# Kernel tuning notes

Hardware: AMD Instinct MI355X
Metric: run time of the kernel (lower is better)

Reference implementation:

```python
import jax, jax.numpy as jnp
import numpy as np

APP_DIM = 27
FEA_PE = 6
VIEW_PE = 6
FEATURE_C = 128
DENSITY_SHIFT = -10.0
DISTANCE_SCALE = 25.0
IN_MLPC = 2 * VIEW_PE * 3 + 2 * FEA_PE * APP_DIM + 3 + APP_DIM  # 390


def positional_encoding(x, freqs):
    # x: [..., C] -> [..., 2*freqs*C]
    freq_bands = (2.0 ** jnp.arange(freqs)).astype(x.dtype)
    pts = (x[..., None] * freq_bands).reshape(x.shape[:-1] + (freqs * x.shape[-1],))
    return jnp.concatenate([jnp.sin(pts), jnp.cos(pts)], axis=-1)


def alpha2weights(alpha):
    # alpha: [N_rays, N_samples]; last sample forced opaque (as in source)
    alpha = alpha.at[:, -1].set(1.0)
    trans = jnp.concatenate(
        [jnp.ones((alpha.shape[0], 1), alpha.dtype), 1.0 - alpha + 1e-10], axis=-1)
    T = jnp.cumprod(trans, axis=-1)
    weights = alpha * T[:, :-1]
    return weights, T


def setup_inputs() -> dict:
    key = jax.random.key(0)
    ks = jax.random.split(key, 12)
    N_rays, N_samples = 4096, 128
    sigma_feat = jax.random.normal(ks[0], (N_rays, N_samples), jnp.float32)
    app_features = 0.1 * jax.random.normal(ks[1], (N_rays, N_samples, APP_DIM), jnp.float32)
    vd = jax.random.normal(ks[2], (N_rays, N_samples, 3), jnp.float32)
    viewdirs = vd / (jnp.linalg.norm(vd, axis=-1, keepdims=True) + 1e-8)
    dists = 0.02 * jax.random.uniform(ks[3], (N_rays, N_samples), jnp.float32)

    def linear(k, fan_in, fan_out):
        kw, kb = jax.random.split(k)
        lim = 1.0 / np.sqrt(fan_in)
        W = jax.random.uniform(kw, (fan_in, fan_out), jnp.float32, -lim, lim)
        b = jax.random.uniform(kb, (fan_out,), jnp.float32, -lim, lim)
        return W, b

    W1, b1 = linear(ks[4], IN_MLPC, FEATURE_C)
    W2, b2 = linear(ks[5], FEATURE_C, FEATURE_C)
    W3, _ = linear(ks[6], FEATURE_C, 3)
    b3 = jnp.zeros((3,), jnp.float32)  # bias of last layer initialized to 0 in source
    return {"sigma_feat": sigma_feat, "app_features": app_features,
            "viewdirs": viewdirs, "dists": dists,
            "W1": W1, "b1": b1, "W2": W2, "b2": b2, "W3": W3, "b3": b3}


def reference(sigma_feat, app_features, viewdirs, dists, W1, b1, W2, b2, W3, b3):
    # feature2density: softplus with density_shift
    sigma = jax.nn.softplus(sigma_feat + DENSITY_SHIFT)
    alpha = 1.0 - jnp.exp(-sigma * dists * DISTANCE_SCALE)  # [N_rays, N_samples]
    weights, _T = alpha2weights(alpha)

    # MLPRender_Fea: cat[features, viewdirs, PE(features), PE(viewdirs)]
    mlp_in = jnp.concatenate(
        [app_features, viewdirs,
         positional_encoding(app_features, FEA_PE),
         positional_encoding(viewdirs, VIEW_PE)], axis=-1)  # [R, S, 390]
    h = jax.nn.relu(jnp.einsum('rsc,cf->rsf', mlp_in, W1) + b1)
    h = jax.nn.relu(jnp.einsum('rsf,fg->rsg', h, W2) + b2)
    rgb = jax.nn.sigmoid(jnp.einsum('rsg,go->rso', h, W3) + b3)  # [R, S, 3]

    rgb_map = jnp.sum(weights[..., None] * rgb, axis=-2)  # [R, 3]
    return rgb_map
```

## Files before the change

### kernel.cpp

```cpp
#include <hip/hip_runtime.h>
#include <math.h>

typedef unsigned short u16;
using bf16x8 = __attribute__((ext_vector_type(8))) short;
using f32x4  = __attribute__((ext_vector_type(4))) float;

#define NS      128
#define NBLOCKS 4096
#define NSLICE  19
#define OWGT    81920

#define POOLSZ 32768
#define OH2    16384

#define BAR() do { asm volatile("s_waitcnt lgkmcnt(0)" ::: "memory");        \
                   __builtin_amdgcn_s_barrier();                              \
                   asm volatile("" ::: "memory"); } while (0)

#define MF(A,B,C) __builtin_amdgcn_mfma_f32_16x16x32_bf16((A),(B),(C),0,0,0)

__device__ __forceinline__ u16 f2bf(float f) {
    unsigned int i = __float_as_uint(f);
    return (u16)((i + 0x7FFFu + ((i >> 16) & 1u)) >> 16);
}

__device__ __forceinline__ unsigned pk(float hi, float lo) {
    unsigned r;
    asm("v_cvt_pk_bf16_f32 %0, %1, %2" : "=v"(r) : "v"(lo), "v"(hi));
    return r;
}

__device__ __forceinline__ int afoff_h(int m, int k) {
    int chunk = ((k >> 5) * 8 + (m >> 4)) * 64 + ((k >> 3) & 3) * 16 + (m & 15);
    chunk ^= (k >> 3) & 3;
    return chunk * 8 + (k & 7);
}

__device__ __forceinline__ int orig_k(int ch, int slot) {
    if (ch < 27) {
        if (slot == 0) return ch;
        if (slot <= 6) return 30 + ch * 6 + (slot - 1);
        return 192 + ch * 6 + (slot - 7);
    } else {
        int c = ch - 27;
        if (slot == 0) return 27 + c;
        if (slot <= 6) return 354 + c * 6 + (slot - 1);
        return 372 + c * 6 + (slot - 7);
    }
}

__device__ __forceinline__ float ldch(const float* ap, const float* vp, int c) {
    return (c < 27) ? ap[c] : vp[c - 27];
}

__device__ __forceinline__ void build_x(u16* dst, float v) {
    float rev = v * 0.15915494309189535f;
    rev -= floorf(rev);
    float s0 = __builtin_amdgcn_sinf(rev);
    float c0 = __builtin_amdgcn_cosf(rev);
    float s1 = 2.f * s0 * c0, c1 = c0 * c0 - s0 * s0;
    float s2 = 2.f * s1 * c1, c2 = c1 * c1 - s1 * s1;
    float s3 = 2.f * s2 * c2, c3 = c2 * c2 - s2 * s2;
    float s4 = 2.f * s3 * c3, c4 = c3 * c3 - s3 * s3;
    float s5 = 2.f * s4 * c4, c5 = c4 * c4 - s4 * s4;
    uint4 lo, hi;
    lo.x = pk(s0, v);  lo.y = pk(s2, s1);  lo.z = pk(s4, s3);  lo.w = pk(c0, s5);
    hi.x = pk(c2, c1); hi.y = pk(c4, c3);  hi.z = pk(0.f, c5); hi.w = 0u;
    *(uint4*)(dst)       = lo;
    *(uint4*)(dst + 128) = hi;
}

__global__ __launch_bounds__(256) void prep_kernel(
    const float* __restrict__ W1, const float* __restrict__ W2,
    const float* __restrict__ W3, const float* __restrict__ sigma_g,
    const float* __restrict__ dists_g, u16* __restrict__ ws,
    float* __restrict__ out)
{
    int idx = blockIdx.x * 256 + threadIdx.x;
    if (idx < 12288) out[idx] = 0.f;
    if (idx < 61440) {
        int j = idx & 7, lane = (idx >> 3) & 63, nt = (idx >> 9) & 7, ks = idx >> 12;
        int q = lane >> 4, l15 = lane & 15;
        int klocal = q * 8 + j;
        int ch = ks * 2 + (klocal >> 4);
        int slot = klocal & 15;
        int n = nt * 16 + l15;
        ws[idx] = (slot < 13) ? f2bf(W1[orig_k(ch, slot) * 128 + n]) : (u16)0;
    } else if (idx < 77824) {
        int i2 = idx - 61440;
        int j = i2 & 7, lane = (i2 >> 3) & 63, nt = (i2 >> 9) & 7, ks = i2 >> 12;
        int k = ks * 32 + (lane >> 4) * 8 + j;
        int n = nt * 16 + (lane & 15);
        ws[idx] = f2bf(W2[k * 128 + n]);
    } else if (idx < 79872) {
        int i3 = idx - 77824;
        int j = i3 & 7, lane = (i3 >> 3) & 63, ks = i3 >> 9;
        int k = ks * 32 + (lane >> 4) * 8 + j;
        int n = lane & 15;
        ws[idx] = (n < 3) ? f2bf(W3[k * 3 + n]) : (u16)0;
    }
    {
        int ray = idx >> 6, ln = idx & 63;
        float* wgt = (float*)(ws + OWGT);
        int base = ray * NS;
        float x0 = sigma_g[base + ln] - 10.f;
        float sp0 = (x0 > 20.f) ? x0 : log1pf(expf(x0));
        float a0 = 1.f - expf(-sp0 * dists_g[base + ln] * 25.f);
        float x1 = sigma_g[base + 64 + ln] - 10.f;
        float sp1 = (x1 > 20.f) ? x1 : log1pf(expf(x1));
        float a1 = 1.f - expf(-sp1 * dists_g[base + 64 + ln] * 25.f);
        if (ln == 63) a1 = 1.f;
        float p0 = 1.f - a0 + 1e-10f;
        float p1 = 1.f - a1 + 1e-10f;
        #pragma unroll
        for (int d = 1; d < 64; d <<= 1) {
            float v0 = __shfl_up(p0, d);
            float v1 = __shfl_up(p1, d);
            if (ln >= d) { p0 *= v0; p1 *= v1; }
        }
        float S0 = __shfl(p0, 63);
        float q0 = __shfl_up(p0, 1);
        float q1 = __shfl_up(p1, 1);
        wgt[base + ln]      = a0 * ((ln == 0) ? 1.f : q0);
        wgt[base + 64 + ln] = a1 * ((ln == 0) ? 1.f : q1) * S0;
    }
}

#define LOADB2(N0, N1, s)                                                     \
    if ((s) < NSLICE) {                                                       \
        const u16* wp = wp0 + (s) * 4096;                                     \
        N0 = *(const bf16x8*)(wp);                                            \
        N1 = *(const bf16x8*)(wp + 512);                                      \
    }

#define BODYX(s, C0,C1, N0,N1)                                                \
  {                                                                           \
    LOADB2(N0, N1, (s)+2);                                                    \
    const u16* ab = pool + ((s)&7)*4096 + (wm*256 + lane)*8;                  \
    bf16x8 a0 = *(const bf16x8*)(ab);                                         \
    bf16x8 a1 = *(const bf16x8*)(ab + 512);                                   \
    __builtin_amdgcn_s_setprio(1);                                            \
    acc[0][0]=MF(a0,C0,acc[0][0]); acc[0][1]=MF(a0,C1,acc[0][1]);             \
    acc[1][0]=MF(a1,C0,acc[1][0]); acc[1][1]=MF(a1,C1,acc[1][1]);             \
    a0 = *(const bf16x8*)(ab + 1024);                                         \
    a1 = *(const bf16x8*)(ab + 1536);                                         \
    acc[2][0]=MF(a0,C0,acc[2][0]); acc[2][1]=MF(a0,C1,acc[2][1]);             \
    acc[3][0]=MF(a1,C0,acc[3][0]); acc[3][1]=MF(a1,C1,acc[3][1]);             \
    __builtin_amdgcn_s_setprio(0);                                            \
  }

#define BODYX0(s, C0,C1, N0,N1)                                               \
  {                                                                           \
    LOADB2(N0, N1, (s)+2);                                                    \
    const u16* ab = pool + ((s)&7)*4096 + (wm*256 + lane)*8;                  \
    bf16x8 a0 = *(const bf16x8*)(ab);                                         \
    bf16x8 a1 = *(const bf16x8*)(ab + 512);                                   \
    __builtin_amdgcn_s_setprio(1);                                            \
    acc[0][0]=MF(a0,C0,vzero); acc[0][1]=MF(a0,C1,vzero);                     \
    acc[1][0]=MF(a1,C0,vzero); acc[1][1]=MF(a1,C1,vzero);                     \
    a0 = *(const bf16x8*)(ab + 1024);                                         \
    a1 = *(const bf16x8*)(ab + 1536);                                         \
    acc[2][0]=MF(a0,C0,vzero); acc[2][1]=MF(a0,C1,vzero);                     \
    acc[3][0]=MF(a1,C0,vzero); acc[3][1]=MF(a1,C1,vzero);                     \
    __builtin_amdgcn_s_setprio(0);                                            \
  }

#define BODYH(s, C0,C1, N0,N1)                                                \
  {                                                                           \
    LOADB2(N0, N1, (s)+2);                                                    \
    int cb = ((((s)-15)*512) + wm*256 + lane) ^ quad;                         \
    bf16x8 a0 = *(const bf16x8*)(pool + cb*8);                                \
    bf16x8 a1 = *(const bf16x8*)(pool + (cb+64)*8);                           \
    __builtin_amdgcn_s_setprio(1);                                            \
    acc[0][0]=MF(a0,C0,acc[0][0]); acc[0][1]=MF(a0,C1,acc[0][1]);             \
    acc[1][0]=MF(a1,C0,acc[1][0]); acc[1][1]=MF(a1,C1,acc[1][1]);             \
    a0 = *(const bf16x8*)(pool + (cb+128)*8);                                 \
    a1 = *(const bf16x8*)(pool + (cb+192)*8);                                 \
    acc[2][0]=MF(a0,C0,acc[2][0]); acc[2][1]=MF(a0,C1,acc[2][1]);             \
    acc[3][0]=MF(a1,C0,acc[3][0]); acc[3][1]=MF(a1,C1,acc[3][1]);             \
    __builtin_amdgcn_s_setprio(0);                                            \
  }

#define BODYH0(s, C0,C1, N0,N1)                                               \
  {                                                                           \
    LOADB2(N0, N1, (s)+2);                                                    \
    int cb = ((((s)-15)*512) + wm*256 + lane) ^ quad;                         \
    bf16x8 a0 = *(const bf16x8*)(pool + cb*8);                                \
    bf16x8 a1 = *(const bf16x8*)(pool + (cb+64)*8);                           \
    __builtin_amdgcn_s_setprio(1);                                            \
    acc[0][0]=MF(a0,C0,vzero); acc[0][1]=MF(a0,C1,vzero);                     \
    acc[1][0]=MF(a1,C0,vzero); acc[1][1]=MF(a1,C1,vzero);                     \
    a0 = *(const bf16x8*)(pool + (cb+128)*8);                                 \
    a1 = *(const bf16x8*)(pool + (cb+192)*8);                                 \
    acc[2][0]=MF(a0,C0,vzero); acc[2][1]=MF(a0,C1,vzero);                     \
    acc[3][0]=MF(a1,C0,vzero); acc[3][1]=MF(a1,C1,vzero);                     \
    __builtin_amdgcn_s_setprio(0);                                            \
  }

#define GENDQ(p)                                                              \
  {                                                                           \
    if (8*(p)+8  + cl < 30)                                                   \
        build_x(pool + ((2*(p)+2)&3)*8192 + (cl>>1)*4096 + bxoff, pv_a);      \
    if (8*(p)+12 + cl < 30)                                                   \
        build_x(pool + ((2*(p)+3)&3)*8192 + (cl>>1)*4096 + bxoff, pv_b);      \
    pv_a = pv_c; pv_b = pv_d;                                                 \
    if (8*(p)+24 + cl < 30) pv_c = ldch(ap, vp, 8*(p)+24 + cl);               \
    if (8*(p)+28 + cl < 30) pv_d = ldch(ap, vp, 8*(p)+28 + cl);               \
    BAR();                                                                    \
  }

#define EPI4(OFS, ACC, BB, rwb, col)                                          \
  { f32x4 t_ = ACC + BB;                                                      \
    t_ = __builtin_elementwise_max(t_, vzero);                                \
    unsigned w01_ = pk(t_[1], t_[0]);                                         \
    unsigned w23_ = pk(t_[3], t_[2]);                                         \
    pool[(OFS) + afoff_h((rwb) + 0, col)] = (u16)w01_;                        \
    pool[(OFS) + afoff_h((rwb) + 1, col)] = (u16)(w01_ >> 16);                \
    pool[(OFS) + afoff_h((rwb) + 2, col)] = (u16)w23_;                        \
    pool[(OFS) + afoff_h((rwb) + 3, col)] = (u16)(w23_ >> 16); }

__global__ __launch_bounds__(512, 4) void render_kernel(
    const float* __restrict__ app_g,   const float* __restrict__ view_g,
    const float* __restrict__ b1_g,    const float* __restrict__ b2_g,
    const float* __restrict__ b3_g,    const u16* __restrict__ ws,
    float* __restrict__ out_g)
{
    __shared__ __align__(16) u16 pool[POOLSZ];

    const int tid  = threadIdx.x;
    const int lane = tid & 63;
    const int wave = tid >> 6;
    const int l15  = lane & 15;
    const int quad = lane >> 4;
    const int wm   = wave >> 2;
    const int wn   = wave & 3;

    const int r  = blockIdx.x;
    const int rb = r * NS;
    const int row = tid & 127;
    const int cl  = tid >> 7;
    const float* ap = app_g  + (rb + row) * 27;
    const float* vp = view_g + (rb + row) * 3;
    const int bxoff = (row >> 4) * 512 + (((cl & 1) * 32) + (row & 15)) * 8;

    const u16* wp0 = ws + (wn * 128 + lane) * 8;
    bf16x8 bP0, bP1, bQ0, bQ1, bR0, bR1;
    LOADB2(bP0, bP1, 0);
    LOADB2(bQ0, bQ1, 1);

    float pv_a = ldch(ap, vp, cl);
    float pv_b = ldch(ap, vp, 4 + cl);
    float pv_c = ldch(ap, vp, 8 + cl);
    float pv_d = ldch(ap, vp, 12 + cl);

    build_x(pool +        (cl >> 1) * 4096 + bxoff, pv_a);
    build_x(pool + 8192 + (cl >> 1) * 4096 + bxoff, pv_b);
    pv_a = pv_c; pv_b = pv_d;
    pv_c = ldch(ap, vp, 16 + cl);
    pv_d = ldch(ap, vp, 20 + cl);
    BAR();

    const f32x4 vzero = {0.f, 0.f, 0.f, 0.f};
    f32x4 acc[4][2];

    BODYX0(0, bP0,bP1, bR0,bR1);
    BODYX(1,  bQ0,bQ1, bP0,bP1);
    BODYX(2,  bR0,bR1, bQ0,bQ1);
    BODYX(3,  bP0,bP1, bR0,bR1);  GENDQ(0);
    BODYX(4,  bQ0,bQ1, bP0,bP1);
    BODYX(5,  bR0,bR1, bQ0,bQ1);
    BODYX(6,  bP0,bP1, bR0,bR1);
    BODYX(7,  bQ0,bQ1, bP0,bP1);  GENDQ(1);
    BODYX(8,  bR0,bR1, bQ0,bQ1);
    BODYX(9,  bP0,bP1, bR0,bR1);
    BODYX(10, bQ0,bQ1, bP0,bP1);
    BODYX(11, bR0,bR1, bQ0,bQ1);  GENDQ(2);
    const float b1r0 = b1_g[wn * 32 + l15];
    const float b1r1 = b1_g[wn * 32 + 16 + l15];
    BODYX(12, bP0,bP1, bR0,bR1);
    BODYX(13, bQ0,bQ1, bP0,bP1);
    BODYX(14, bR0,bR1, bQ0,bQ1);

    {
        const f32x4 bb0 = {b1r0, b1r0, b1r0, b1r0};
        const f32x4 bb1 = {b1r1, b1r1, b1r1, b1r1};
        #pragma unroll
        for (int mt = 0; mt < 4; ++mt) {
            int rwb = wm * 64 + mt * 16 + quad * 4;
            EPI4(0, acc[mt][0], bb0, rwb, wn * 32 + l15);
            EPI4(0, acc[mt][1], bb1, rwb, wn * 32 + 16 + l15);
        }
    }
    BAR();

    const float b2r0 = b2_g[wn * 32 + l15];
    const float b2r1 = b2_g[wn * 32 + 16 + l15];

    BODYH0(15, bP0,bP1, bR0,bR1);
    BODYH(16, bQ0,bQ1, bP0,bP1);
    BODYH(17, bR0,bR1, bQ0,bQ1);
    BODYH(18, bP0,bP1, bR0,bR1);

    {
        const f32x4 bb0 = {b2r0, b2r0, b2r0, b2r0};
        const f32x4 bb1 = {b2r1, b2r1, b2r1, b2r1};
        #pragma unroll
        for (int mt = 0; mt < 4; ++mt) {
            int rwb = wm * 64 + mt * 16 + quad * 4;
            EPI4(OH2, acc[mt][0], bb0, rwb, wn * 32 + l15);
            EPI4(OH2, acc[mt][1], bb1, rwb, wn * 32 + 16 + l15);
        }
    }
    BAR();

    const u16* w3r = ws + 77824;
    const float4 w4 = *(const float4*)((const float*)(ws + OWGT)
                                       + rb + wave * 16 + quad * 4);
    const float b3v = (l15 < 3) ? b3_g[l15] : 0.f;
    f32x4 acc3 = vzero;
    #pragma unroll
    for (int ks = 0; ks < 4; ++ks) {
        bf16x8 w3f = *(const bf16x8*)(w3r + (ks * 64 + lane) * 8);
        int c = ((ks * 8 + wave) * 64 + lane) ^ quad;
        bf16x8 a3 = *(const bf16x8*)(pool + OH2 + c * 8);
        acc3 = MF(a3, w3f, acc3);
    }
    float v = 0.f;
    if (l15 < 3) {
        v  = w4.x / (1.f + expf(-(acc3[0] + b3v)));
        v += w4.y / (1.f + expf(-(acc3[1] + b3v)));
        v += w4.z / (1.f + expf(-(acc3[2] + b3v)));
        v += w4.w / (1.f + expf(-(acc3[3] + b3v)));
    }
    v += __shfl_xor(v, 16);
    v += __shfl_xor(v, 32);
    if (lane < 3)
        atomicAdd(&out_g[r * 3 + lane], v);
}

extern "C" void kernel_launch(void* const* d_in, const int* in_sizes, int n_in,
                              void* d_out, int out_size, void* d_ws, size_t ws_size,
                              hipStream_t stream) {
    (void)in_sizes; (void)n_in; (void)out_size; (void)ws_size;
    const float* sigma = (const float*)d_in[0];
    const float* app   = (const float*)d_in[1];
    const float* view  = (const float*)d_in[2];
    const float* dists = (const float*)d_in[3];
    const float* W1    = (const float*)d_in[4];
    const float* b1    = (const float*)d_in[5];
    const float* W2    = (const float*)d_in[6];
    const float* b2    = (const float*)d_in[7];
    const float* W3    = (const float*)d_in[8];
    const float* b3    = (const float*)d_in[9];
    float* out = (float*)d_out;

    u16* ws = (u16*)d_ws;

    prep_kernel<<<1024, 256, 0, stream>>>(W1, W2, W3, sigma, dists, ws, out);
    render_kernel<<<NBLOCKS, 512, 0, stream>>>(app, view, b1, b2, b3, ws, out);
}
```

Baseline: 192.9 us.

## Process four rays per block with cross-ray prefetch of inputs and weights

Turns the kernel into a persistent-style loop where each block handles four consecutive rays instead of one, launching a quarter as many blocks. The next ray's feature and viewdir loads are issued mid-way through the current ray's first GEMM, and the next x tile is built in shared memory after the final layer. This amortizes block launch and prologue cost and overlaps global loads with MFMA work. In exchange there are fewer blocks (1024) for load balance across CUs, plus an extra barrier per ray. Correctness depends on the macros still reading pv_* and pool state consistently across iterations.

After: 375.5 us. 94.6% more time.

```diff
diff --git a/kernel.cpp b/kernel.cpp
--- a/kernel.cpp
+++ b/kernel.cpp
@@ -6,7 +6,8 @@
 using f32x4  = __attribute__((ext_vector_type(4))) float;
 
 #define NS      128
-#define NBLOCKS 4096
+#define RPB     4
+#define NBLOCKS (4096 / RPB)
 #define NSLICE  19
 #define OWGT    81920
 
@@ -235,13 +236,12 @@
     const int wm   = wave >> 2;
     const int wn   = wave & 3;
 
-    const int r  = blockIdx.x;
-    const int rb = r * NS;
-    const int row = tid & 127;
-    const int cl  = tid >> 7;
-    const float* ap = app_g  + (rb + row) * 27;
-    const float* vp = view_g + (rb + row) * 3;
-    const int bxoff = (row >> 4) * 512 + (((cl & 1) * 32) + (row & 15)) * 8;
+    const int r0  = blockIdx.x * RPB;
+    const int rowl = tid & 127;
+    const int cl   = tid >> 7;
+    const float* ap = app_g  + (r0 * NS + rowl) * 27;
+    const float* vp = view_g + (r0 * NS + rowl) * 3;
+    const int bxoff = (rowl >> 4) * 512 + (((cl & 1) * 32) + (rowl & 15)) * 8;
 
     const u16* wp0 = ws + (wn * 128 + lane) * 8;
     bf16x8 bP0, bP1, bQ0, bQ1, bR0, bR1;
@@ -261,81 +261,103 @@
     BAR();
 
     const f32x4 vzero = {0.f, 0.f, 0.f, 0.f};
+    const u16* w3r = ws + 77824;
+    const float b3v = (l15 < 3) ? b3_g[l15] : 0.f;
     f32x4 acc[4][2];
 
-    BODYX0(0, bP0,bP1, bR0,bR1);
-    BODYX(1,  bQ0,bQ1, bP0,bP1);
-    BODYX(2,  bR0,bR1, bQ0,bQ1);
-    BODYX(3,  bP0,bP1, bR0,bR1);  GENDQ(0);
-    BODYX(4,  bQ0,bQ1, bP0,bP1);
-    BODYX(5,  bR0,bR1, bQ0,bQ1);
-    BODYX(6,  bP0,bP1, bR0,bR1);
-    BODYX(7,  bQ0,bQ1, bP0,bP1);  GENDQ(1);
-    BODYX(8,  bR0,bR1, bQ0,bQ1);
-    BODYX(9,  bP0,bP1, bR0,bR1);
-    BODYX(10, bQ0,bQ1, bP0,bP1);
-    BODYX(11, bR0,bR1, bQ0,bQ1);  GENDQ(2);
-    const float b1r0 = b1_g[wn * 32 + l15];
-    const float b1r1 = b1_g[wn * 32 + 16 + l15];
-    BODYX(12, bP0,bP1, bR0,bR1);
-    BODYX(13, bQ0,bQ1, bP0,bP1);
-    BODYX(14, bR0,bR1, bQ0,bQ1);
-
-    {
-        const f32x4 bb0 = {b1r0, b1r0, b1r0, b1r0};
-        const f32x4 bb1 = {b1r1, b1r1, b1r1, b1r1};
+    #pragma unroll 1
+    for (int ri = 0; ri < RPB; ++ri) {
+        BODYX0(0, bP0,bP1, bR0,bR1);
+        BODYX(1,  bQ0,bQ1, bP0,bP1);
+        BODYX(2,  bR0,bR1, bQ0,bQ1);
+        BODYX(3,  bP0,bP1, bR0,bR1);  GENDQ(0);
+        BODYX(4,  bQ0,bQ1, bP0,bP1);
+        BODYX(5,  bR0,bR1, bQ0,bQ1);
+        BODYX(6,  bP0,bP1, bR0,bR1);
+        BODYX(7,  bQ0,bQ1, bP0,bP1);  GENDQ(1);
+        BODYX(8,  bR0,bR1, bQ0,bQ1);
+        BODYX(9,  bP0,bP1, bR0,bR1);
+        BODYX(10, bQ0,bQ1, bP0,bP1);
+        BODYX(11, bR0,bR1, bQ0,bQ1);  GENDQ(2);
+
+        if (ri + 1 < RPB) {
+            ap += NS * 27; vp += NS * 3;
+            pv_a = ldch(ap, vp, cl);
+            pv_b = ldch(ap, vp, 4 + cl);
+            pv_c = ldch(ap, vp, 8 + cl);
+            pv_d = ldch(ap, vp, 12 + cl);
+        }
+        const float b1r0 = b1_g[wn * 32 + l15];
+        const float b1r1 = b1_g[wn * 32 + 16 + l15];
+        BODYX(12, bP0,bP1, bR0,bR1);
+        BODYX(13, bQ0,bQ1, bP0,bP1);
+        BODYX(14, bR0,bR1, bQ0,bQ1);
+
+        {
+            const f32x4 bb0 = {b1r0, b1r0, b1r0, b1r0};
+            const f32x4 bb1 = {b1r1, b1r1, b1r1, b1r1};
+            #pragma unroll
+            for (int mt = 0; mt < 4; ++mt) {
+                int rwb = wm * 64 + mt * 16 + quad * 4;
+                EPI4(0, acc[mt][0], bb0, rwb, wn * 32 + l15);
+                EPI4(0, acc[mt][1], bb1, rwb, wn * 32 + 16 + l15);
+            }
+        }
+        BAR();
+
+        const float b2r0 = b2_g[wn * 32 + l15];
+        const float b2r1 = b2_g[wn * 32 + 16 + l15];
+
+        BODYH0(15, bP0,bP1, bR0,bR1);
+        BODYH(16, bQ0,bQ1, bP0,bP1);
+        BODYH(17, bR0,bR1, bQ0,bQ1);
+        BODYH(18, bP0,bP1, bR0,bR1);
+
+        {
+            const f32x4 bb0 = {b2r0, b2r0, b2r0, b2r0};
+            const f32x4 bb1 = {b2r1, b2r1, b2r1, b2r1};
+            #pragma unroll
+            for (int mt = 0; mt < 4; ++mt) {
+                int rwb = wm * 64 + mt * 16 + quad * 4;
+                EPI4(OH2, acc[mt][0], bb0, rwb, wn * 32 + l15);
+                EPI4(OH2, acc[mt][1], bb1, rwb, wn * 32 + 16 + l15);
+            }
+        }
+        BAR();
+
+        const float4 w4 = *(const float4*)((const float*)(ws + OWGT)
+                          + (r0 + ri) * NS + wave * 16 + quad * 4);
+        f32x4 acc3 = vzero;
         #pragma unroll
-        for (int mt = 0; mt < 4; ++mt) {
-            int rwb = wm * 64 + mt * 16 + quad * 4;
-            EPI4(0, acc[mt][0], bb0, rwb, wn * 32 + l15);
-            EPI4(0, acc[mt][1], bb1, rwb, wn * 32 + 16 + l15);
-        }
-    }
-    BAR();
-
-    const float b2r0 = b2_g[wn * 32 + l15];
-    const float b2r1 = b2_g[wn * 32 + 16 + l15];
-
-    BODYH0(15, bP0,bP1, bR0,bR1);
-    BODYH(16, bQ0,bQ1, bP0,bP1);
-    BODYH(17, bR0,bR1, bQ0,bQ1);
-    BODYH(18, bP0,bP1, bR0,bR1);
-
-    {
-        const f32x4 bb0 = {b2r0, b2r0, b2r0, b2r0};
-        const f32x4 bb1 = {b2r1, b2r1, b2r1, b2r1};
-        #pragma unroll
-        for (int mt = 0; mt < 4; ++mt) {
-            int rwb = wm * 64 + mt * 16 + quad * 4;
-            EPI4(OH2, acc[mt][0], bb0, rwb, wn * 32 + l15);
-            EPI4(OH2, acc[mt][1], bb1, rwb, wn * 32 + 16 + l15);
-        }
-    }
-    BAR();
-
-    const u16* w3r = ws + 77824;
-    const float4 w4 = *(const float4*)((const float*)(ws + OWGT)
-                                       + rb + wave * 16 + quad * 4);
-    const float b3v = (l15 < 3) ? b3_g[l15] : 0.f;
-    f32x4 acc3 = vzero;
-    #pragma unroll
-    for (int ks = 0; ks < 4; ++ks) {
-        bf16x8 w3f = *(const bf16x8*)(w3r + (ks * 64 + lane) * 8);
-        int c = ((ks * 8 + wave) * 64 + lane) ^ quad;
-        bf16x8 a3 = *(const bf16x8*)(pool + OH2 + c * 8);
-        acc3 = MF(a3, w3f, acc3);
-    }
-    float v = 0.f;
-    if (l15 < 3) {
-        v  = w4.x / (1.f + expf(-(acc3[0] + b3v)));
-        v += w4.y / (1.f + expf(-(acc3[1] + b3v)));
-        v += w4.z / (1.f + expf(-(acc3[2] + b3v)));
-        v += w4.w / (1.f + expf(-(acc3[3] + b3v)));
-    }
-    v += __shfl_xor(v, 16);
-    v += __shfl_xor(v, 32);
-    if (lane < 3)
-        atomicAdd(&out_g[r * 3 + lane], v);
+        for (int ks = 0; ks < 4; ++ks) {
+            bf16x8 w3f = *(const bf16x8*)(w3r + (ks * 64 + lane) * 8);
+            int c = ((ks * 8 + wave) * 64 + lane) ^ quad;
+            bf16x8 a3 = *(const bf16x8*)(pool + OH2 + c * 8);
+            acc3 = MF(a3, w3f, acc3);
+        }
+        if (ri + 1 < RPB) {
+            LOADB2(bP0, bP1, 0);
+            LOADB2(bQ0, bQ1, 1);
+            build_x(pool +        (cl >> 1) * 4096 + bxoff, pv_a);
+            build_x(pool + 8192 + (cl >> 1) * 4096 + bxoff, pv_b);
+            pv_a = pv_c; pv_b = pv_d;
+            pv_c = ldch(ap, vp, 16 + cl);
+            pv_d = ldch(ap, vp, 20 + cl);
+        }
+        float v = 0.f;
+        if (l15 < 3) {
+            v  = w4.x / (1.f + expf(-(acc3[0] + b3v)));
+            v += w4.y / (1.f + expf(-(acc3[1] + b3v)));
+            v += w4.z / (1.f + expf(-(acc3[2] + b3v)));
+            v += w4.w / (1.f + expf(-(acc3[3] + b3v)));
+        }
+        v += __shfl_xor(v, 16);
+        v += __shfl_xor(v, 32);
+        if (lane < 3)
+            atomicAdd(&out_g[(r0 + ri) * 3 + lane], v);
+
+        if (ri + 1 < RPB) BAR();
+    }
 }
 
 extern "C" void kernel_launch(void* const* d_in, const int* in_sizes, int n_in,
```

## Process two rays per block with cross-ray prefetch of inputs and weights

Applied to the files above, without the earlier changes.

Each block now handles two rays in sequence instead of one, halving the grid. While the first ray is still in its later layers, the block prefetches the second ray's input features and weight fragments and builds its first encoded input tiles. This hides per-block startup latency and overlaps it with the previous ray's epilogue. The cost is more register pressure and half as many blocks, which leaves fewer blocks to balance across CUs.

Measured after the change: 235.0 us. 21.8% more time.

```diff
diff --git a/kernel.cpp b/kernel.cpp
--- a/kernel.cpp
+++ b/kernel.cpp
@@ -6,7 +6,8 @@
 using f32x4  = __attribute__((ext_vector_type(4))) float;
 
 #define NS      128
-#define NBLOCKS 4096
+#define RPB     2
+#define NBLOCKS (4096 / RPB)
 #define NSLICE  19
 #define OWGT    81920
 
@@ -219,6 +220,95 @@
     pool[(OFS) + afoff_h((rwb) + 2, col)] = (u16)w23_;                        \
     pool[(OFS) + afoff_h((rwb) + 3, col)] = (u16)(w23_ >> 16); }
 
+#define RAY(RI, PREF)                                                         \
+  {                                                                           \
+    BODYX0(0, bP0,bP1, bR0,bR1);                              \
+    BODYX(1,  bQ0,bQ1, bP0,bP1);                                              \
+    BODYX(2,  bR0,bR1, bQ0,bQ1);                                              \
+    BODYX(3,  bP0,bP1, bR0,bR1);  GENDQ(0);           \
+    BODYX(4,  bQ0,bQ1, bP0,bP1);                                              \
+    BODYX(5,  bR0,bR1, bQ0,bQ1);                                              \
+    BODYX(6,  bP0,bP1, bR0,bR1);                                              \
+    BODYX(7,  bQ0,bQ1, bP0,bP1);  GENDQ(1);          \
+    BODYX(8,  bR0,bR1, bQ0,bQ1);                                              \
+    BODYX(9,  bP0,bP1, bR0,bR1);                                              \
+    BODYX(10, bQ0,bQ1, bP0,bP1);                                              \
+    BODYX(11, bR0,bR1, bQ0,bQ1);  GENDQ(2);         \
+    if (PREF) {   \
+        ap += NS * 27; vp += NS * 3;                                          \
+        pv_a = ldch(ap, vp, cl);                                              \
+        pv_b = ldch(ap, vp, 4 + cl);                                          \
+        pv_c = ldch(ap, vp, 8 + cl);                                          \
+        pv_d = ldch(ap, vp, 12 + cl);                                         \
+    }                                                                         \
+    const float b1r0 = b1_g[wn * 32 + l15];                                   \
+    const float b1r1 = b1_g[wn * 32 + 16 + l15];                              \
+    BODYX(12, bP0,bP1, bR0,bR1);                                              \
+    BODYX(13, bQ0,bQ1, bP0,bP1);                     \
+    BODYX(14, bR0,bR1, bQ0,bQ1);                     \
+        \
+    {                                                                         \
+        const f32x4 bb0 = {b1r0, b1r0, b1r0, b1r0};                           \
+        const f32x4 bb1 = {b1r1, b1r1, b1r1, b1r1};                           \
+        _Pragma("unroll")                                                     \
+        for (int mt = 0; mt < 4; ++mt) {                                      \
+            int rwb = wm * 64 + mt * 16 + quad * 4;                           \
+            EPI4(0, acc[mt][0], bb0, rwb, wn * 32 + l15);                     \
+            EPI4(0, acc[mt][1], bb1, rwb, wn * 32 + 16 + l15);                \
+        }                                                                     \
+    }                                                                         \
+    BAR();                           \
+    const float b2r0 = b2_g[wn * 32 + l15];                                   \
+    const float b2r1 = b2_g[wn * 32 + 16 + l15];                              \
+    BODYH0(15, bP0,bP1, bR0,bR1);              \
+    BODYH(16, bQ0,bQ1, bP0,bP1);                     \
+    BODYH(17, bR0,bR1, bQ0,bQ1);                                              \
+    BODYH(18, bP0,bP1, bR0,bR1);                                              \
+        \
+    {                                                                         \
+        const f32x4 bb0 = {b2r0, b2r0, b2r0, b2r0};                           \
+        const f32x4 bb1 = {b2r1, b2r1, b2r1, b2r1};                           \
+        _Pragma("unroll")                                                     \
+        for (int mt = 0; mt < 4; ++mt) {                                      \
+            int rwb = wm * 64 + mt * 16 + quad * 4;                           \
+            EPI4(OH2, acc[mt][0], bb0, rwb, wn * 32 + l15);                   \
+            EPI4(OH2, acc[mt][1], bb1, rwb, wn * 32 + 16 + l15);              \
+        }                                                                     \
+    }                                                                         \
+    BAR();                  \
+       \
+    const float4 w4 = *(const float4*)((const float*)(ws + OWGT)              \
+                      + (r0 + (RI)) * NS + wave * 16 + quad * 4);             \
+    f32x4 acc3 = vzero;                                                       \
+    _Pragma("unroll")                                                         \
+    for (int ks = 0; ks < 4; ++ks) {                                          \
+        bf16x8 w3f = *(const bf16x8*)(w3r + (ks * 64 + lane) * 8);            \
+        int c = ((ks * 8 + wave) * 64 + lane) ^ quad;                         \
+        bf16x8 a3 = *(const bf16x8*)(pool + OH2 + c * 8);                     \
+        acc3 = MF(a3, w3f, acc3);                                             \
+    }                                                                         \
+    if (PREF) {                                                               \
+        LOADB2(bP0, bP1, 0);                  \
+        LOADB2(bQ0, bQ1, 1);                                                  \
+        build_x(pool +        (cl >> 1) * 4096 + bxoff, pv_a);                \
+        build_x(pool + 8192 + (cl >> 1) * 4096 + bxoff, pv_b);                \
+        pv_a = pv_c; pv_b = pv_d;                                             \
+        pv_c = ldch(ap, vp, 16 + cl);                                 \
+        pv_d = ldch(ap, vp, 20 + cl);                                 \
+    }                                                                         \
+    float v = 0.f;                                                            \
+    if (l15 < 3) {                                                            \
+        v  = w4.x / (1.f + expf(-(acc3[0] + b3v)));                           \
+        v += w4.y / (1.f + expf(-(acc3[1] + b3v)));                           \
+        v += w4.z / (1.f + expf(-(acc3[2] + b3v)));                           \
+        v += w4.w / (1.f + expf(-(acc3[3] + b3v)));                           \
+    }                                                                         \
+    v += __shfl_xor(v, 16);                                                   \
+    v += __shfl_xor(v, 32);                                                   \
+    if (lane < 3)                                                             \
+        atomicAdd(&out_g[(r0 + (RI)) * 3 + lane], v);                         \
+  }
+
 __global__ __launch_bounds__(512, 4) void render_kernel(
     const float* __restrict__ app_g,   const float* __restrict__ view_g,
     const float* __restrict__ b1_g,    const float* __restrict__ b2_g,
@@ -235,13 +325,12 @@
     const int wm   = wave >> 2;
     const int wn   = wave & 3;
 
-    const int r  = blockIdx.x;
-    const int rb = r * NS;
-    const int row = tid & 127;
-    const int cl  = tid >> 7;
-    const float* ap = app_g  + (rb + row) * 27;
-    const float* vp = view_g + (rb + row) * 3;
-    const int bxoff = (row >> 4) * 512 + (((cl & 1) * 32) + (row & 15)) * 8;
+    const int r0  = blockIdx.x * RPB;
+    const int rowl = tid & 127;
+    const int cl   = tid >> 7;
+    const float* ap = app_g  + (r0 * NS + rowl) * 27;
+    const float* vp = view_g + (r0 * NS + rowl) * 3;
+    const int bxoff = (rowl >> 4) * 512 + (((cl & 1) * 32) + (rowl & 15)) * 8;
 
     const u16* wp0 = ws + (wn * 128 + lane) * 8;
     bf16x8 bP0, bP1, bQ0, bQ1, bR0, bR1;
@@ -261,81 +350,13 @@
     BAR();
 
     const f32x4 vzero = {0.f, 0.f, 0.f, 0.f};
+    const u16* w3r = ws + 77824;
+    const float b3v = (l15 < 3) ? b3_g[l15] : 0.f;
     f32x4 acc[4][2];
 
-    BODYX0(0, bP0,bP1, bR0,bR1);
-    BODYX(1,  bQ0,bQ1, bP0,bP1);
-    BODYX(2,  bR0,bR1, bQ0,bQ1);
-    BODYX(3,  bP0,bP1, bR0,bR1);  GENDQ(0);
-    BODYX(4,  bQ0,bQ1, bP0,bP1);
-    BODYX(5,  bR0,bR1, bQ0,bQ1);
-    BODYX(6,  bP0,bP1, bR0,bR1);
-    BODYX(7,  bQ0,bQ1, bP0,bP1);  GENDQ(1);
-    BODYX(8,  bR0,bR1, bQ0,bQ1);
-    BODYX(9,  bP0,bP1, bR0,bR1);
-    BODYX(10, bQ0,bQ1, bP0,bP1);
-    BODYX(11, bR0,bR1, bQ0,bQ1);  GENDQ(2);
-    const float b1r0 = b1_g[wn * 32 + l15];
-    const float b1r1 = b1_g[wn * 32 + 16 + l15];
-    BODYX(12, bP0,bP1, bR0,bR1);
-    BODYX(13, bQ0,bQ1, bP0,bP1);
-    BODYX(14, bR0,bR1, bQ0,bQ1);
-
-    {
-        const f32x4 bb0 = {b1r0, b1r0, b1r0, b1r0};
-        const f32x4 bb1 = {b1r1, b1r1, b1r1, b1r1};
-        #pragma unroll
-        for (int mt = 0; mt < 4; ++mt) {
-            int rwb = wm * 64 + mt * 16 + quad * 4;
-            EPI4(0, acc[mt][0], bb0, rwb, wn * 32 + l15);
-            EPI4(0, acc[mt][1], bb1, rwb, wn * 32 + 16 + l15);
-        }
-    }
+    RAY(0, 1);
     BAR();
-
-    const float b2r0 = b2_g[wn * 32 + l15];
-    const float b2r1 = b2_g[wn * 32 + 16 + l15];
-
-    BODYH0(15, bP0,bP1, bR0,bR1);
-    BODYH(16, bQ0,bQ1, bP0,bP1);
-    BODYH(17, bR0,bR1, bQ0,bQ1);
-    BODYH(18, bP0,bP1, bR0,bR1);
-
-    {
-        const f32x4 bb0 = {b2r0, b2r0, b2r0, b2r0};
-        const f32x4 bb1 = {b2r1, b2r1, b2r1, b2r1};
-        #pragma unroll
-        for (int mt = 0; mt < 4; ++mt) {
-            int rwb = wm * 64 + mt * 16 + quad * 4;
-            EPI4(OH2, acc[mt][0], bb0, rwb, wn * 32 + l15);
-            EPI4(OH2, acc[mt][1], bb1, rwb, wn * 32 + 16 + l15);
-        }
-    }
-    BAR();
-
-    const u16* w3r = ws + 77824;
-    const float4 w4 = *(const float4*)((const float*)(ws + OWGT)
-                                       + rb + wave * 16 + quad * 4);
-    const float b3v = (l15 < 3) ? b3_g[l15] : 0.f;
-    f32x4 acc3 = vzero;
-    #pragma unroll
-    for (int ks = 0; ks < 4; ++ks) {
-        bf16x8 w3f = *(const bf16x8*)(w3r + (ks * 64 + lane) * 8);
-        int c = ((ks * 8 + wave) * 64 + lane) ^ quad;
-        bf16x8 a3 = *(const bf16x8*)(pool + OH2 + c * 8);
-        acc3 = MF(a3, w3f, acc3);
-    }
-    float v = 0.f;
-    if (l15 < 3) {
-        v  = w4.x / (1.f + expf(-(acc3[0] + b3v)));
-        v += w4.y / (1.f + expf(-(acc3[1] + b3v)));
-        v += w4.z / (1.f + expf(-(acc3[2] + b3v)));
-        v += w4.w / (1.f + expf(-(acc3[3] + b3v)));
-    }
-    v += __shfl_xor(v, 16);
-    v += __shfl_xor(v, 32);
-    if (lane < 3)
-        atomicAdd(&out_g[r * 3 + lane], v);
+    RAY(1, 0);
 }
 
 extern "C" void kernel_launch(void* const* d_in, const int* in_sizes, int n_in,
```
